# Kernel tuning notes

Measured on AMD Instinct MI355X. Metric: run time of the kernel, lower is better.

## Reference

```python
import jax, jax.numpy as jnp
from jax import lax
import numpy as np

B, L_IN, C_IN, C_MARK = 4, 1024, 7, 4
D, H, DK, DFF, NL = 512, 8, 64, 2048, 4
WINDOW = [4, 4, 4]
INNER = 5


def _get_mask(input_size, window_size, inner_size):
    all_size = [input_size]
    for w in window_size:
        all_size.append(all_size[-1] // w)
    L = sum(all_size)
    m = np.zeros((L, L), dtype=np.float32)
    iw = inner_size // 2
    for li in range(len(all_size)):
        start = sum(all_size[:li])
        for i in range(start, start + all_size[li]):
            m[i, max(i - iw, start):min(i + iw + 1, start + all_size[li])] = 1
    for li in range(1, len(all_size)):
        start = sum(all_size[:li])
        for i in range(start, start + all_size[li]):
            ls = start - all_size[li - 1] + (i - start) * window_size[li - 1]
            if i == start + all_size[li] - 1:
                rs = start
            else:
                rs = start - all_size[li - 1] + (i - start + 1) * window_size[li - 1]
            m[i, ls:rs] = 1
            m[ls:rs, i] = 1
    return (1 - m).astype(bool), all_size


def _refer_points(all_sizes, window_size):
    n = all_sizes[0]
    idx = np.zeros((n, len(all_sizes)), dtype=np.int64)
    for i in range(n):
        idx[i, 0] = i
        former = i
        for j in range(1, len(all_sizes)):
            start = sum(all_sizes[:j])
            inner = former - (start - all_sizes[j - 1])
            former = start + min(inner // window_size[j - 1], all_sizes[j] - 1)
            idx[i, j] = former
    return idx


def _pos_emb(L, d):
    pos = np.arange(L, dtype=np.float32)[:, None]
    div = np.exp(np.arange(0, d, 2, dtype=np.float32) * (-np.log(10000.0) / d))
    pe = np.zeros((L, d), dtype=np.float32)
    pe[:, 0::2] = np.sin(pos * div)
    pe[:, 1::2] = np.cos(pos * div)
    return pe


def _ln(x, g, b, eps=1e-5):
    mu = x.mean(-1, keepdims=True)
    v = ((x - mu) ** 2).mean(-1, keepdims=True)
    return (x - mu) * lax.rsqrt(v + eps) * g + b


def setup_inputs() -> dict:
    key = jax.random.key(0)
    ks = iter(jax.random.split(key, 64))

    def nrm(shape, fan_in):
        return jax.random.normal(next(ks), shape, jnp.float32) / np.float32(np.sqrt(fan_in))

    return dict(
        x_enc=jax.random.normal(next(ks), (B, L_IN, C_IN), jnp.float32),
        x_mark=jax.random.uniform(next(ks), (B, L_IN, C_MARK), jnp.float32),
        conv_w=nrm((D, C_IN, 3), C_IN * 3), conv_b=jnp.zeros((D,), jnp.float32),
        temp_w=nrm((C_MARK, D), C_MARK), temp_b=jnp.zeros((D,), jnp.float32),
        down_w=nrm((D, DK), D), down_b=jnp.zeros((DK,), jnp.float32),
        pyr_conv_w=nrm((3, DK, DK, WINDOW[0]), DK * WINDOW[0]),
        pyr_conv_b=jnp.zeros((3, DK), jnp.float32),
        bn_g=jnp.ones((3, DK), jnp.float32), bn_b=jnp.zeros((3, DK), jnp.float32),
        up_w=nrm((DK, D), DK), up_b=jnp.zeros((D,), jnp.float32),
        norm_g=jnp.ones((D,), jnp.float32), norm_b=jnp.zeros((D,), jnp.float32),
        wq=nrm((NL, D, H * DK), D), wk=nrm((NL, D, H * DK), D), wv=nrm((NL, D, H * DK), D),
        fc_w=nrm((NL, H * DK, D), H * DK), fc_b=jnp.zeros((NL, D), jnp.float32),
        ln1_g=jnp.ones((NL, D), jnp.float32), ln1_b=jnp.zeros((NL, D), jnp.float32),
        w1=nrm((NL, D, DFF), D), b1=jnp.zeros((NL, DFF), jnp.float32),
        w2=nrm((NL, DFF, D), DFF), b2=jnp.zeros((NL, D), jnp.float32),
        ln2_g=jnp.ones((NL, D), jnp.float32), ln2_b=jnp.zeros((NL, D), jnp.float32),
    )


def reference(x_enc, x_mark, conv_w, conv_b, temp_w, temp_b, down_w, down_b,
              pyr_conv_w, pyr_conv_b, bn_g, bn_b, up_w, up_b, norm_g, norm_b,
              wq, wk, wv, fc_w, fc_b, ln1_g, ln1_b, w1, b1, w2, b2, ln2_g, ln2_b):
    mask_np, all_size = _get_mask(L_IN, WINDOW, INNER)
    mask = jnp.asarray(mask_np)                      # (L_tot, L_tot) bool, True = blocked
    idx = jnp.asarray(_refer_points(all_size, WINDOW))  # (L_IN, n_levels)
    pe = jnp.asarray(_pos_emb(L_IN, D))
    L_tot = sum(all_size)

    # --- DataEmbedding: circular Conv1d token emb + positional + temporal linear ---
    xt = jnp.transpose(x_enc, (0, 2, 1))             # (B, C_IN, L)
    xt = jnp.concatenate([xt[:, :, -1:], xt, xt[:, :, :1]], axis=-1)  # circular pad=1
    val = lax.conv_general_dilated(xt, conv_w, (1,), 'VALID',
                                   dimension_numbers=('NCH', 'OIH', 'NCH'))
    val = jnp.transpose(val, (0, 2, 1)) + conv_b
    seq = val + pe[None] + x_mark @ temp_w + temp_b  # (B, L_IN, D); dropout = eval no-op

    # --- Bottleneck_Construct: build pyramid levels with strided convs ---
    tmp = jnp.transpose(seq @ down_w + down_b, (0, 2, 1))  # (B, DK, L_IN)
    outs = []
    for i in range(len(WINDOW)):
        tmp = lax.conv_general_dilated(tmp, pyr_conv_w[i], (WINDOW[i],), 'VALID',
                                       dimension_numbers=('NCH', 'OIH', 'NCH'))
        tmp = tmp + pyr_conv_b[i][None, :, None]
        # BatchNorm1d at eval with running stats (0,1): affine only
        tmp = jax.nn.elu(tmp * bn_g[i][None, :, None] + bn_b[i][None, :, None])
        outs.append(tmp)
    pyr = jnp.transpose(jnp.concatenate(outs, axis=2), (0, 2, 1)) @ up_w + up_b
    seq = _ln(jnp.concatenate([seq, pyr], axis=1), norm_g, norm_b)  # (B, L_tot, D)

    temperature = float(np.sqrt(DK))
    for l in range(NL):
        # post-norm multi-head attention with pyramidal boolean mask
        res = seq
        q = (seq @ wq[l]).reshape(B, L_tot, H, DK)
        k = (seq @ wk[l]).reshape(B, L_tot, H, DK)
        v = (seq @ wv[l]).reshape(B, L_tot, H, DK)
        att = jnp.einsum('bqhd,bkhd->bhqk', q / temperature, k)
        att = jnp.where(mask[None, None], jnp.float32(-1e9), att)
        p = jax.nn.softmax(att, axis=-1)
        o = jnp.einsum('bhqk,bkhd->bqhd', p, v).reshape(B, L_tot, H * DK)
        seq = _ln(o @ fc_w[l] + fc_b[l] + res, ln1_g[l], ln1_b[l])
        # post-norm FFN (exact gelu, as F.gelu)
        res = seq
        hmid = jax.nn.gelu(seq @ w1[l] + b1[l], approximate=False)
        seq = _ln(hmid @ w2[l] + b2[l] + res, ln2_g[l], ln2_b[l])

    # --- refer_points gather: concat all pyramid levels per input position ---
    out = seq[:, idx, :]                             # (B, L_IN, n_levels, D)
    return out.reshape(B, L_IN, -1)                  # (B, L_IN, n_levels*D)
```

## Files before the change

### kernel.cpp

```cpp
#include <hip/hip_runtime.h>
#include <hip/hip_bf16.h>
#include <math.h>


typedef __attribute__((ext_vector_type(8))) short short8;
typedef __attribute__((ext_vector_type(4))) float f32x4;

__device__ inline ushort f2bf(float x) {
  union { __hip_bfloat16 h; ushort u; } cv; cv.h = __float2bfloat16(x); return cv.u;
}
__device__ inline float bf2f(ushort u) {
  union { unsigned int i; float f; } cv; cv.i = (unsigned)u << 16; return cv.f;
}
__device__ inline float lo16(unsigned u) { union { unsigned i; float f; } c; c.i = u << 16; return c.f; }
__device__ inline float hi16(unsigned u) { union { unsigned i; float f; } c; c.i = u & 0xffff0000u; return c.f; }
__device__ inline unsigned pack2(float a, float b) {
  return (unsigned)f2bf(a) | ((unsigned)f2bf(b) << 16);
}

__device__ inline float gelu_f(float x) {
  float y = 0.7978845608028654f * (x + 0.044715f * x * x * x);
  float t = __expf(-2.0f * y);
  float th = (1.0f - t) / (1.0f + t);
  return 0.5f * x * (1.0f + th);
}

__device__ inline int xcd_chunk(int orig, int nwg) {
  int q = nwg >> 3, r = nwg & 7;
  int xcd = orig & 7, idx = orig >> 3;
  int base = (xcd < r) ? xcd * (q + 1) : r * (q + 1) + (xcd - r) * q;
  return base + idx;
}

#define GLD16(gp, lp)                                                        \
  __builtin_amdgcn_global_load_lds(                                          \
      (const __attribute__((address_space(1))) void*)(gp),                   \
      (__attribute__((address_space(3))) void*)(lp), 16, 0, 0)

__global__ __launch_bounds__(512) void embed_kernel(
    const float* __restrict__ x_enc, const float* __restrict__ x_mark,
    const float* __restrict__ conv_w, const float* __restrict__ conv_b,
    const float* __restrict__ temp_w, const float* __restrict__ temp_b,
    float* __restrict__ e) {
  int bl = blockIdx.x;
  int b = bl >> 10, l = bl & 1023;
  int d = threadIdx.x;
  int lm1 = (l + 1023) & 1023;
  int lp1 = (l + 1) & 1023;
  const float* w  = conv_w + d * 21;
  const float* x0 = x_enc + (size_t)(b * 1024 + lm1) * 7;
  const float* x1 = x_enc + (size_t)(b * 1024 + l)   * 7;
  const float* x2 = x_enc + (size_t)(b * 1024 + lp1) * 7;
  float acc = conv_b[d];
#pragma unroll
  for (int ci = 0; ci < 7; ci++) {
    acc = fmaf(x0[ci], w[ci * 3 + 0], acc);
    acc = fmaf(x1[ci], w[ci * 3 + 1], acc);
    acc = fmaf(x2[ci], w[ci * 3 + 2], acc);
  }
  int j = d >> 1;
  float dv = expf((float)(2 * j) * (-9.210340371976184f / 512.0f));
  float ang = (float)l * dv;
  float pe = (d & 1) ? cosf(ang) : sinf(ang);
  const float* xm = x_mark + (size_t)(b * 1024 + l) * 4;
  float mk = temp_b[d];
  mk = fmaf(xm[0], temp_w[d],        mk);
  mk = fmaf(xm[1], temp_w[512 + d],  mk);
  mk = fmaf(xm[2], temp_w[1024 + d], mk);
  mk = fmaf(xm[3], temp_w[1536 + d], mk);
  e[(size_t)bl * 512 + d] = acc + pe + mk;
}

__global__ __launch_bounds__(256) void transpose_cast(
    const float* __restrict__ src, ushort* __restrict__ dst,
    int K, int N, size_t src_lstride, size_t dst_lstride) {
  src += (size_t)blockIdx.z * src_lstride;
  dst += (size_t)blockIdx.z * dst_lstride;
  __shared__ float t[32][33];
  int k0 = blockIdx.y * 32, n0 = blockIdx.x * 32;
  int tx = threadIdx.x, ty = threadIdx.y;
#pragma unroll
  for (int i = 0; i < 4; i++)
    t[ty + i * 8][tx] = src[(size_t)(k0 + ty + i * 8) * N + n0 + tx];
  __syncthreads();
#pragma unroll
  for (int i = 0; i < 4; i++)
    dst[(size_t)(n0 + ty + i * 8) * K + k0 + tx] = f2bf(t[tx][ty + i * 8]);
}

__global__ __launch_bounds__(256) void gemm_bf16_t64(
    const ushort* __restrict__ A, const ushort* __restrict__ Bt,
    const float* __restrict__ bias, ushort* __restrict__ C,
    int N, int K, int act) {
  __shared__ short As[2][4096];
  __shared__ short Bs[2][4096];
  int nbx = N >> 6;
  int wgid = xcd_chunk(blockIdx.x, gridDim.x);
  int bx = wgid % nbx, by = wgid / nbx;
  int tid = threadIdx.x;
  int w = tid >> 6, lane = tid & 63;
  int bm = by << 6, bn = bx << 6;
  int gch = (tid & 7) ^ ((tid >> 3) & 7);
  const short* Ab = (const short*)A + (size_t)(bm + (tid >> 3)) * K + gch * 8;
  const short* Bb = (const short*)Bt + (size_t)(bn + (tid >> 3)) * K + gch * 8;
  int ldst = (tid & 192) * 8;
  int wr = (w >> 1) << 5, wc = (w & 1) << 5;
  int lr = lane & 15, kg = lane >> 4;
  int cs0 = ((kg)     ^ (lane & 7)) * 8;
  int cs1 = ((4 + kg) ^ (lane & 7)) * 8;
  f32x4 acc[2][2] = {};
#define STG64(buf, kt) do {                                                  \
    GLD16(Ab + (kt),                  &As[buf][ldst]);                       \
    GLD16(Ab + (kt) + (size_t)32 * K, &As[buf][2048 + ldst]);                \
    GLD16(Bb + (kt),                  &Bs[buf][ldst]);                       \
    GLD16(Bb + (kt) + (size_t)32 * K, &Bs[buf][2048 + ldst]); } while (0)
  STG64(0, 0);
  __syncthreads();
  int nt = K >> 6;
  for (int t = 0; t < nt; t++) {
    int cur = t & 1;
    if (t + 1 < nt) STG64(cur ^ 1, (t + 1) << 6);
    short8 a_[2][2], b_[2][2];
#pragma unroll
    for (int m = 0; m < 2; m++) {
      int rb = (wr + m * 16 + lr) * 64;
      a_[m][0] = *(const short8*)&As[cur][rb + cs0];
      a_[m][1] = *(const short8*)&As[cur][rb + cs1];
    }
#pragma unroll
    for (int n = 0; n < 2; n++) {
      int rb = (wc + n * 16 + lr) * 64;
      b_[n][0] = *(const short8*)&Bs[cur][rb + cs0];
      b_[n][1] = *(const short8*)&Bs[cur][rb + cs1];
    }
#pragma unroll
    for (int ks = 0; ks < 2; ks++)
#pragma unroll
      for (int m = 0; m < 2; m++)
#pragma unroll
        for (int n = 0; n < 2; n++)
          acc[m][n] = __builtin_amdgcn_mfma_f32_16x16x32_bf16(a_[m][ks], b_[n][ks], acc[m][n], 0, 0, 0);
    __syncthreads();
  }
#undef STG64
  int r0 = bm + wr + kg * 4;
  int c0 = bn + wc + lr;
#pragma unroll
  for (int m = 0; m < 2; m++) {
#pragma unroll
    for (int n = 0; n < 2; n++) {
      int col = c0 + n * 16;
      float bv = bias ? bias[col] : 0.0f;
#pragma unroll
      for (int j = 0; j < 4; j++) {
        int row = r0 + m * 16 + j;
        float v = acc[m][n][j] + bv;
        if (act == 1) v = gelu_f(v);
        C[(size_t)row * N + col] = f2bf(v);
      }
    }
  }
}

__global__ __launch_bounds__(256) void gemm_bf16_t32(
    const ushort* __restrict__ A, const ushort* __restrict__ Bt,
    const float* __restrict__ bias, ushort* __restrict__ C,
    int N, int K) {
  __shared__ short As[2][2048];
  __shared__ short Bs[2][4096];
  int nbx = N >> 6;
  int wgid = xcd_chunk(blockIdx.x, gridDim.x);
  int bx = wgid % nbx, by = wgid / nbx;
  int tid = threadIdx.x;
  int w = tid >> 6, lane = tid & 63;
  int bm = by << 5, bn = bx << 6;
  int gch = (tid & 7) ^ ((tid >> 3) & 7);
  const short* Ab = (const short*)A + (size_t)(bm + (tid >> 3)) * K + gch * 8;
  const short* Bb = (const short*)Bt + (size_t)(bn + (tid >> 3)) * K + gch * 8;
  int ldst = (tid & 192) * 8;
  int wr = (w >> 1) << 4, wc = (w & 1) << 5;
  int lr = lane & 15, kg = lane >> 4;
  int cs0 = ((kg)     ^ (lane & 7)) * 8;
  int cs1 = ((4 + kg) ^ (lane & 7)) * 8;
  f32x4 acc[2] = {};
#define STG32(buf, kt) do {                                                  \
    GLD16(Ab + (kt),                  &As[buf][ldst]);                       \
    GLD16(Bb + (kt),                  &Bs[buf][ldst]);                       \
    GLD16(Bb + (kt) + (size_t)32 * K, &Bs[buf][2048 + ldst]); } while (0)
  STG32(0, 0);
  __syncthreads();
  int nt = K >> 6;
  for (int t = 0; t < nt; t++) {
    int cur = t & 1;
    if (t + 1 < nt) STG32(cur ^ 1, (t + 1) << 6);
    short8 a_[2], b_[2][2];
    {
      int rb = (wr + lr) * 64;
      a_[0] = *(const short8*)&As[cur][rb + cs0];
      a_[1] = *(const short8*)&As[cur][rb + cs1];
    }
#pragma unroll
    for (int n = 0; n < 2; n++) {
      int rb = (wc + n * 16 + lr) * 64;
      b_[n][0] = *(const short8*)&Bs[cur][rb + cs0];
      b_[n][1] = *(const short8*)&Bs[cur][rb + cs1];
    }
#pragma unroll
    for (int ks = 0; ks < 2; ks++)
#pragma unroll
      for (int n = 0; n < 2; n++)
        acc[n] = __builtin_amdgcn_mfma_f32_16x16x32_bf16(a_[ks], b_[n][ks], acc[n], 0, 0, 0);
    __syncthreads();
  }
#undef STG32
  int r0 = bm + wr + kg * 4;
  int c0 = bn + wc + lr;
#pragma unroll
  for (int n = 0; n < 2; n++) {
    int col = c0 + n * 16;
    float bv = bias ? bias[col] : 0.0f;
#pragma unroll
    for (int j = 0; j < 4; j++) {
      int row = r0 + j;
      C[(size_t)row * N + col] = f2bf(acc[n][j] + bv);
    }
  }
}

__global__ __launch_bounds__(256) void down_gemm(
    const float* __restrict__ A, const float* __restrict__ B,
    const float* __restrict__ bias, float* __restrict__ C) {
  int wgid = xcd_chunk(blockIdx.x, gridDim.x);
  int r0 = wgid << 4;
  int tid = threadIdx.x;
  int col = tid & 63, rq = tid >> 6;
  __shared__ float As[16][32];
  __shared__ float Bs[32][64];
  float acc0 = 0, acc1 = 0, acc2 = 0, acc3 = 0;
  for (int kt = 0; kt < 512; kt += 32) {
    {
      int e = tid * 2;
      int ar = e >> 5, ak = e & 31;
      *(float2*)&As[ar][ak] = *(const float2*)&A[(size_t)(r0 + ar) * 512 + kt + ak];
    }
    {
      int e = tid * 8;
      int br = e >> 6, bc = e & 63;
      *(float4*)&Bs[br][bc]     = *(const float4*)&B[(size_t)(kt + br) * 64 + bc];
      *(float4*)&Bs[br][bc + 4] = *(const float4*)&B[(size_t)(kt + br) * 64 + bc + 4];
    }
    __syncthreads();
#pragma unroll
    for (int kk = 0; kk < 32; kk++) {
      float bv = Bs[kk][col];
      acc0 = fmaf(As[rq][kk],      bv, acc0);
      acc1 = fmaf(As[rq + 4][kk],  bv, acc1);
      acc2 = fmaf(As[rq + 8][kk],  bv, acc2);
      acc3 = fmaf(As[rq + 12][kk], bv, acc3);
    }
    __syncthreads();
  }
  float bv = bias[col];
  C[(size_t)(r0 + rq) * 64 + col]      = acc0 + bv;
  C[(size_t)(r0 + rq + 4) * 64 + col]  = acc1 + bv;
  C[(size_t)(r0 + rq + 8) * 64 + col]  = acc2 + bv;
  C[(size_t)(r0 + rq + 12) * 64 + col] = acc3 + bv;
}

__global__ __launch_bounds__(256) void gemm_f32(
    const float* __restrict__ A, const float* __restrict__ B,
    const float* __restrict__ bias, float* __restrict__ C,
    int M, int N, int K) {
  __shared__ float As[16][68];
  __shared__ float Bs[16][64];
  int tid = threadIdx.x;
  int tx = tid & 15, ty = tid >> 4;
  int bm = blockIdx.y << 6, bn = blockIdx.x << 6;
  const float* Ab = A + (size_t)bm * K;
  const float* Bb = B + bn;
  float acc[4][4] = {};
  for (int kt = 0; kt < K; kt += 16) {
#pragma unroll
    for (int r = 0; r < 4; r++) {
      int e2 = r * 256 + tid;
      As[e2 & 15][e2 >> 4] = Ab[(size_t)(e2 >> 4) * K + kt + (e2 & 15)];
    }
#pragma unroll
    for (int r = 0; r < 4; r++) {
      int e2 = r * 256 + tid;
      Bs[e2 >> 6][e2 & 63] = Bb[(size_t)(kt + (e2 >> 6)) * N + (e2 & 63)];
    }
    __syncthreads();
#pragma unroll
    for (int kk = 0; kk < 16; kk++) {
      float a0 = As[kk][(ty << 2) + 0], a1 = As[kk][(ty << 2) + 1];
      float a2 = As[kk][(ty << 2) + 2], a3 = As[kk][(ty << 2) + 3];
      float b0 = Bs[kk][(tx << 2) + 0], b1 = Bs[kk][(tx << 2) + 1];
      float b2 = Bs[kk][(tx << 2) + 2], b3 = Bs[kk][(tx << 2) + 3];
      acc[0][0] = fmaf(a0, b0, acc[0][0]); acc[0][1] = fmaf(a0, b1, acc[0][1]);
      acc[0][2] = fmaf(a0, b2, acc[0][2]); acc[0][3] = fmaf(a0, b3, acc[0][3]);
      acc[1][0] = fmaf(a1, b0, acc[1][0]); acc[1][1] = fmaf(a1, b1, acc[1][1]);
      acc[1][2] = fmaf(a1, b2, acc[1][2]); acc[1][3] = fmaf(a1, b3, acc[1][3]);
      acc[2][0] = fmaf(a2, b0, acc[2][0]); acc[2][1] = fmaf(a2, b1, acc[2][1]);
      acc[2][2] = fmaf(a2, b2, acc[2][2]); acc[2][3] = fmaf(a2, b3, acc[2][3]);
      acc[3][0] = fmaf(a3, b0, acc[3][0]); acc[3][1] = fmaf(a3, b1, acc[3][1]);
      acc[3][2] = fmaf(a3, b2, acc[3][2]); acc[3][3] = fmaf(a3, b3, acc[3][3]);
    }
    __syncthreads();
  }
#pragma unroll
  for (int i2 = 0; i2 < 4; i2++) {
    int row = bm + (ty << 2) + i2;
#pragma unroll
    for (int j2 = 0; j2 < 4; j2++) {
      int col = bn + (tx << 2) + j2;
      C[(size_t)row * N + col] = acc[i2][j2] + (bias ? bias[col] : 0.0f);
    }
  }
}

__global__ __launch_bounds__(64) void pyr_conv(
    const float* __restrict__ in, int in_base, int in_bstr,
    float* __restrict__ out, int out_base, int out_bstr, int out_len,
    const float* __restrict__ w, const float* __restrict__ bias,
    const float* __restrict__ bng, const float* __restrict__ bnb) {
  int blk = blockIdx.x;
  int b = blk / out_len, to = blk - b * out_len;
  int co = threadIdx.x;
  __shared__ float xin[4][64];
  const float* src = in + (size_t)(b * in_bstr + in_base + 4 * to) * 64;
#pragma unroll
  for (int r2 = 0; r2 < 4; r2++) xin[r2][co] = src[r2 * 64 + co];
  __syncthreads();
  const float* wr = w + (size_t)co * 256;
  float acc = bias[co];
#pragma unroll 16
  for (int ci = 0; ci < 64; ci++) {
    acc = fmaf(xin[0][ci], wr[ci * 4 + 0], acc);
    acc = fmaf(xin[1][ci], wr[ci * 4 + 1], acc);
    acc = fmaf(xin[2][ci], wr[ci * 4 + 2], acc);
    acc = fmaf(xin[3][ci], wr[ci * 4 + 3], acc);
  }
  float y = fmaf(bng[co], acc, bnb[co]);
  y = y > 0.0f ? y : expm1f(y);
  out[(size_t)(b * out_bstr + out_base + to) * 64 + co] = y;
}

__global__ __launch_bounds__(256) void ln_concat(
    const float* __restrict__ e, const float* __restrict__ pyru,
    const float* __restrict__ g, const float* __restrict__ bta,
    ushort* __restrict__ seq_bf) {
  int r = (blockIdx.x << 2) + (threadIdx.x >> 6);
  int lane = threadIdx.x & 63;
  int b = r / 1360, i = r - b * 1360;
  const float* src = (i < 1024)
      ? (e    + (size_t)(b * 1024 + i) * 512)
      : (pyru + (size_t)(b * 336 + (i - 1024)) * 512);
  int c = lane << 3;
  float4 v0 = *(const float4*)&src[c];
  float4 v1 = *(const float4*)&src[c + 4];
  float sum = v0.x + v0.y + v0.z + v0.w + v1.x + v1.y + v1.z + v1.w;
#pragma unroll
  for (int off = 1; off < 64; off <<= 1) sum += __shfl_xor(sum, off);
  float mu = sum * (1.0f / 512.0f);
  float d[8] = { v0.x - mu, v0.y - mu, v0.z - mu, v0.w - mu,
                 v1.x - mu, v1.y - mu, v1.z - mu, v1.w - mu };
  float sq = d[0]*d[0] + d[1]*d[1] + d[2]*d[2] + d[3]*d[3]
           + d[4]*d[4] + d[5]*d[5] + d[6]*d[6] + d[7]*d[7];
#pragma unroll
  for (int off = 1; off < 64; off <<= 1) sq += __shfl_xor(sq, off);
  float inv = rsqrtf(sq * (1.0f / 512.0f) + 1e-5f);
  float4 g0 = *(const float4*)&g[c],   g1 = *(const float4*)&g[c + 4];
  float4 b0 = *(const float4*)&bta[c], b1 = *(const float4*)&bta[c + 4];
  uint4 pk;
  pk.x = pack2(d[0]*inv*g0.x + b0.x, d[1]*inv*g0.y + b0.y);
  pk.y = pack2(d[2]*inv*g0.z + b0.z, d[3]*inv*g0.w + b0.w);
  pk.z = pack2(d[4]*inv*g1.x + b1.x, d[5]*inv*g1.y + b1.y);
  pk.w = pack2(d[6]*inv*g1.z + b1.z, d[7]*inv*g1.w + b1.w);
  *(uint4*)(seq_bf + (size_t)r * 512 + c) = pk;
}

__global__ __launch_bounds__(256) void ln_add(
    ushort* __restrict__ seq_bf, const ushort* __restrict__ t1,
    const float* __restrict__ g, const float* __restrict__ bta) {
  int r = (blockIdx.x << 2) + (threadIdx.x >> 6);
  int lane = threadIdx.x & 63;
  int c = lane << 3;
  ushort* row = seq_bf + (size_t)r * 512 + c;
  uint4 sv = *(const uint4*)row;
  uint4 tv = *(const uint4*)(t1 + (size_t)r * 512 + c);
  float v[8] = {
    lo16(sv.x) + lo16(tv.x), hi16(sv.x) + hi16(tv.x),
    lo16(sv.y) + lo16(tv.y), hi16(sv.y) + hi16(tv.y),
    lo16(sv.z) + lo16(tv.z), hi16(sv.z) + hi16(tv.z),
    lo16(sv.w) + lo16(tv.w), hi16(sv.w) + hi16(tv.w) };
  float sum = v[0]+v[1]+v[2]+v[3]+v[4]+v[5]+v[6]+v[7];
#pragma unroll
  for (int off = 1; off < 64; off <<= 1) sum += __shfl_xor(sum, off);
  float mu = sum * (1.0f / 512.0f);
  float sq = 0.0f;
#pragma unroll
  for (int k = 0; k < 8; k++) { v[k] -= mu; sq += v[k] * v[k]; }
#pragma unroll
  for (int off = 1; off < 64; off <<= 1) sq += __shfl_xor(sq, off);
  float inv = rsqrtf(sq * (1.0f / 512.0f) + 1e-5f);
  float4 g0 = *(const float4*)&g[c],   g1 = *(const float4*)&g[c + 4];
  float4 b0 = *(const float4*)&bta[c], b1 = *(const float4*)&bta[c + 4];
  uint4 pk;
  pk.x = pack2(v[0]*inv*g0.x + b0.x, v[1]*inv*g0.y + b0.y);
  pk.y = pack2(v[2]*inv*g0.z + b0.z, v[3]*inv*g0.w + b0.w);
  pk.z = pack2(v[4]*inv*g1.x + b1.x, v[5]*inv*g1.y + b1.y);
  pk.w = pack2(v[6]*inv*g1.z + b1.z, v[7]*inv*g1.w + b1.w);
  *(uint4*)row = pk;
}

__global__ __launch_bounds__(512) void attn_sparse(
    const ushort* __restrict__ qkv, ushort* __restrict__ o) {
  int r = blockIdx.x;
  int b = r / 1360, i = r - b * 1360;
  int h = threadIdx.x >> 6, lane = threadIdx.x & 63;
  int S, sz, li;
  if (i < 1024)      { li = 0; S = 0;    sz = 1024; }
  else if (i < 1280) { li = 1; S = 1024; sz = 256; }
  else if (i < 1344) { li = 2; S = 1280; sz = 64; }
  else               { li = 3; S = 1344; sz = 16; }
  int p = i - S;
  int lo = p - 2; if (lo < 0) lo = 0;
  int hi = p + 2; if (hi > sz - 1) hi = sz - 1;
  int cnt = hi - lo + 1;
  int nk = cnt + (li > 0 ? 4 : 0) + (li < 3 ? 1 : 0);
  int Sprev = (li == 1) ? 0 : (li == 2) ? 1024 : 1280;
  int Snext = (li == 0) ? 1024 : (li == 1) ? 1280 : 1344;
  int j2 = lane >> 2, c = lane & 3;
  int key;
  if (j2 < cnt)                      key = S + lo + j2;
  else if (li > 0 && j2 - cnt < 4)   key = Sprev + 4 * p + (j2 - cnt);
  else if (li < 3)                   key = Snext + (p >> 2);
  else                               key = S + p;
  float partial = 0.0f;
  {
    const uint4* qv = (const uint4*)(qkv + (size_t)r * 1536 + h * 64 + c * 16);
    const uint4* kv = (const uint4*)(qkv + (size_t)(b * 1360 + key) * 1536 + 512 + h * 64 + c * 16);
#pragma unroll
    for (int cc = 0; cc < 2; cc++) {
      uint4 a = qv[cc], k4 = kv[cc];
      partial = fmaf(lo16(a.x), lo16(k4.x), partial); partial = fmaf(hi16(a.x), hi16(k4.x), partial);
      partial = fmaf(lo16(a.y), lo16(k4.y), partial); partial = fmaf(hi16(a.y), hi16(k4.y), partial);
      partial = fmaf(lo16(a.z), lo16(k4.z), partial); partial = fmaf(hi16(a.z), hi16(k4.z), partial);
      partial = fmaf(lo16(a.w), lo16(k4.w), partial); partial = fmaf(hi16(a.w), hi16(k4.w), partial);
    }
  }
  partial += __shfl_xor(partial, 1);
  partial += __shfl_xor(partial, 2);
  float s = partial * 0.125f;
  float m = -1e30f;
  for (int j = 0; j < nk; j++) m = fmaxf(m, __shfl(s, 4 * j));
  float denom = 0.0f;
  for (int j = 0; j < nk; j++) denom += __expf(__shfl(s, 4 * j) - m);
  float inv = 1.0f / denom;
  float acc = 0.0f;
  for (int j = 0; j < nk; j++) {
    float pj = __expf(__shfl(s, 4 * j) - m) * inv;
    int kj = __shfl(key, 4 * j);
    float vv = bf2f(qkv[(size_t)(b * 1360 + kj) * 1536 + 1024 + h * 64 + lane]);
    acc = fmaf(pj, vv, acc);
  }
  o[(size_t)r * 512 + h * 64 + lane] = f2bf(acc);
}

__global__ __launch_bounds__(512) void gather_out(
    const ushort* __restrict__ seq_bf, float* __restrict__ out) {
  int bl = blockIdx.x;
  int b = bl >> 10, i = bl & 1023;
  int d = threadIdx.x;
  size_t ob = (size_t)bl * 2048 + d;
  size_t base = (size_t)b * 1360;
  out[ob]        = bf2f(seq_bf[(base + i) * 512 + d]);
  out[ob + 512]  = bf2f(seq_bf[(base + 1024 + (i >> 2)) * 512 + d]);
  out[ob + 1024] = bf2f(seq_bf[(base + 1280 + (i >> 4)) * 512 + d]);
  out[ob + 1536] = bf2f(seq_bf[(base + 1344 + (i >> 6)) * 512 + d]);
}

extern "C" void kernel_launch(void* const* d_in, const int* in_sizes, int n_in,
                              void* d_out, int out_size, void* d_ws, size_t ws_size,
                              hipStream_t stream) {
  const float* x_enc   = (const float*)d_in[0];
  const float* x_mark  = (const float*)d_in[1];
  const float* conv_w  = (const float*)d_in[2];
  const float* conv_b  = (const float*)d_in[3];
  const float* temp_w  = (const float*)d_in[4];
  const float* temp_b  = (const float*)d_in[5];
  const float* down_w  = (const float*)d_in[6];
  const float* down_b  = (const float*)d_in[7];
  const float* pyr_w   = (const float*)d_in[8];
  const float* pyr_b   = (const float*)d_in[9];
  const float* bn_g    = (const float*)d_in[10];
  const float* bn_b    = (const float*)d_in[11];
  const float* up_w    = (const float*)d_in[12];
  const float* up_b    = (const float*)d_in[13];
  const float* norm_g  = (const float*)d_in[14];
  const float* norm_b  = (const float*)d_in[15];
  const float* wq      = (const float*)d_in[16];
  const float* wk      = (const float*)d_in[17];
  const float* wv      = (const float*)d_in[18];
  const float* fc_w    = (const float*)d_in[19];
  const float* fc_b    = (const float*)d_in[20];
  const float* ln1_g   = (const float*)d_in[21];
  const float* ln1_b   = (const float*)d_in[22];
  const float* w1      = (const float*)d_in[23];
  const float* b1      = (const float*)d_in[24];
  const float* w2      = (const float*)d_in[25];
  const float* b2      = (const float*)d_in[26];
  const float* ln2_g   = (const float*)d_in[27];
  const float* ln2_b   = (const float*)d_in[28];

  float* ws = (float*)d_ws;
  float*  e      = ws;
  float*  tmp0   = ws + 2097152;
  float*  pyrf   = ws + 2359296;
  float*  pyru   = ws + 2445312;
  ushort* qkv_bf = (ushort*)ws;
  ushort* o_bf   = (ushort*)(ws + 4227072);
  ushort* th_bf  = (ushort*)ws;
  ushort* t1     = (ushort*)(ws + 5636096);
  ushort* seq_bf = (ushort*)(ws + 11272192);
  ushort* qkvw   = (ushort*)(ws + 12681216);
  ushort* fcw    = (ushort*)(ws + 14254080);
  ushort* w1t    = (ushort*)(ws + 14778368);
  ushort* w2t    = (ushort*)(ws + 16875520);

  dim3 tb(32, 8);
  transpose_cast<<<dim3(16, 16, 4), tb, 0, stream>>>(wq, qkvw,          512, 512,  262144, 786432);
  transpose_cast<<<dim3(16, 16, 4), tb, 0, stream>>>(wk, qkvw + 262144, 512, 512,  262144, 786432);
  transpose_cast<<<dim3(16, 16, 4), tb, 0, stream>>>(wv, qkvw + 524288, 512, 512,  262144, 786432);
  transpose_cast<<<dim3(16, 16, 4), tb, 0, stream>>>(fc_w, fcw,         512, 512,  262144, 262144);
  transpose_cast<<<dim3(64, 16, 4), tb, 0, stream>>>(w1, w1t,           512, 2048, 1048576, 1048576);
  transpose_cast<<<dim3(16, 64, 4), tb, 0, stream>>>(w2, w2t,           2048, 512, 1048576, 1048576);

  embed_kernel<<<4096, 512, 0, stream>>>(x_enc, x_mark, conv_w, conv_b,
                                         temp_w, temp_b, e);
  down_gemm<<<256, 256, 0, stream>>>(e, down_w, down_b, tmp0);
  pyr_conv<<<4 * 256, 64, 0, stream>>>(tmp0, 0, 1024, pyrf, 0, 336, 256,
                                       pyr_w, pyr_b, bn_g, bn_b);
  pyr_conv<<<4 * 64, 64, 0, stream>>>(pyrf, 0, 336, pyrf, 256, 336, 64,
                                      pyr_w + 16384, pyr_b + 64, bn_g + 64, bn_b + 64);
  pyr_conv<<<4 * 16, 64, 0, stream>>>(pyrf, 256, 336, pyrf, 320, 336, 16,
                                      pyr_w + 32768, pyr_b + 128, bn_g + 128, bn_b + 128);
  gemm_f32<<<dim3(8, 21), 256, 0, stream>>>(pyrf, up_w, up_b, pyru, 1344, 512, 64);
  ln_concat<<<1360, 256, 0, stream>>>(e, pyru, norm_g, norm_b, seq_bf);

  for (int l = 0; l < 4; l++) {
    gemm_bf16_t64<<<24 * 86, 256, 0, stream>>>(seq_bf, qkvw + (size_t)l * 786432,
                                               nullptr, qkv_bf, 1536, 512, 0);
    attn_sparse<<<5440, 512, 0, stream>>>(qkv_bf, o_bf);
    gemm_bf16_t32<<<8 * 172, 256, 0, stream>>>(o_bf, fcw + (size_t)l * 262144,
                                               fc_b + l * 512, t1, 512, 512);
    ln_add<<<1360, 256, 0, stream>>>(seq_bf, t1, ln1_g + l * 512, ln1_b + l * 512);
    gemm_bf16_t64<<<32 * 86, 256, 0, stream>>>(seq_bf, w1t + (size_t)l * 1048576,
                                               b1 + l * 2048, th_bf, 2048, 512, 1);
    gemm_bf16_t32<<<8 * 172, 256, 0, stream>>>(th_bf, w2t + (size_t)l * 1048576,
                                               b2 + l * 512, t1, 512, 2048);
    ln_add<<<1360, 256, 0, stream>>>(seq_bf, t1, ln2_g + l * 512, ln2_b + l * 512);
  }
  gather_out<<<4096, 512, 0, stream>>>(seq_bf, (float*)d_out);
}
```

Baseline: 566.9 us.

## Move pyramid down/up projections to bf16 MFMA GEMMs with bf16 intermediates

Replaces the scalar fp32 down-projection and up-projection GEMMs with the existing bf16 MFMA GEMM kernel. The embedding kernel now also emits a bf16 copy, the pyramid conv stages read and write bf16, and two extra transpose-cast launches prepare the small weights. This removes slow FP32 CUDA-core GEMMs and halves intermediate traffic in the pyramid branch, at the cost of bf16 precision in that branch and two more small launches.

After: 541.8 us. 1.05x faster.

```diff
diff --git a/kernel.cpp b/kernel.cpp
--- a/kernel.cpp
+++ b/kernel.cpp
@@ -41,7 +41,7 @@
     const float* __restrict__ x_enc, const float* __restrict__ x_mark,
     const float* __restrict__ conv_w, const float* __restrict__ conv_b,
     const float* __restrict__ temp_w, const float* __restrict__ temp_b,
-    float* __restrict__ e) {
+    float* __restrict__ e, ushort* __restrict__ e_bf) {
   int bl = blockIdx.x;
   int b = bl >> 10, l = bl & 1023;
   int d = threadIdx.x;
@@ -68,7 +68,9 @@
   mk = fmaf(xm[1], temp_w[512 + d],  mk);
   mk = fmaf(xm[2], temp_w[1024 + d], mk);
   mk = fmaf(xm[3], temp_w[1536 + d], mk);
-  e[(size_t)bl * 512 + d] = acc + pe + mk;
+  float v = acc + pe + mk;
+  e[(size_t)bl * 512 + d] = v;
+  e_bf[(size_t)bl * 512 + d] = f2bf(v);
 }
 
 __global__ __launch_bounds__(256) void transpose_cast(
@@ -227,110 +229,18 @@
   }
 }
 
-__global__ __launch_bounds__(256) void down_gemm(
-    const float* __restrict__ A, const float* __restrict__ B,
-    const float* __restrict__ bias, float* __restrict__ C) {
-  int wgid = xcd_chunk(blockIdx.x, gridDim.x);
-  int r0 = wgid << 4;
-  int tid = threadIdx.x;
-  int col = tid & 63, rq = tid >> 6;
-  __shared__ float As[16][32];
-  __shared__ float Bs[32][64];
-  float acc0 = 0, acc1 = 0, acc2 = 0, acc3 = 0;
-  for (int kt = 0; kt < 512; kt += 32) {
-    {
-      int e = tid * 2;
-      int ar = e >> 5, ak = e & 31;
-      *(float2*)&As[ar][ak] = *(const float2*)&A[(size_t)(r0 + ar) * 512 + kt + ak];
-    }
-    {
-      int e = tid * 8;
-      int br = e >> 6, bc = e & 63;
-      *(float4*)&Bs[br][bc]     = *(const float4*)&B[(size_t)(kt + br) * 64 + bc];
-      *(float4*)&Bs[br][bc + 4] = *(const float4*)&B[(size_t)(kt + br) * 64 + bc + 4];
-    }
-    __syncthreads();
-#pragma unroll
-    for (int kk = 0; kk < 32; kk++) {
-      float bv = Bs[kk][col];
-      acc0 = fmaf(As[rq][kk],      bv, acc0);
-      acc1 = fmaf(As[rq + 4][kk],  bv, acc1);
-      acc2 = fmaf(As[rq + 8][kk],  bv, acc2);
-      acc3 = fmaf(As[rq + 12][kk], bv, acc3);
-    }
-    __syncthreads();
-  }
-  float bv = bias[col];
-  C[(size_t)(r0 + rq) * 64 + col]      = acc0 + bv;
-  C[(size_t)(r0 + rq + 4) * 64 + col]  = acc1 + bv;
-  C[(size_t)(r0 + rq + 8) * 64 + col]  = acc2 + bv;
-  C[(size_t)(r0 + rq + 12) * 64 + col] = acc3 + bv;
-}
-
-__global__ __launch_bounds__(256) void gemm_f32(
-    const float* __restrict__ A, const float* __restrict__ B,
-    const float* __restrict__ bias, float* __restrict__ C,
-    int M, int N, int K) {
-  __shared__ float As[16][68];
-  __shared__ float Bs[16][64];
-  int tid = threadIdx.x;
-  int tx = tid & 15, ty = tid >> 4;
-  int bm = blockIdx.y << 6, bn = blockIdx.x << 6;
-  const float* Ab = A + (size_t)bm * K;
-  const float* Bb = B + bn;
-  float acc[4][4] = {};
-  for (int kt = 0; kt < K; kt += 16) {
-#pragma unroll
-    for (int r = 0; r < 4; r++) {
-      int e2 = r * 256 + tid;
-      As[e2 & 15][e2 >> 4] = Ab[(size_t)(e2 >> 4) * K + kt + (e2 & 15)];
-    }
-#pragma unroll
-    for (int r = 0; r < 4; r++) {
-      int e2 = r * 256 + tid;
-      Bs[e2 >> 6][e2 & 63] = Bb[(size_t)(kt + (e2 >> 6)) * N + (e2 & 63)];
-    }
-    __syncthreads();
-#pragma unroll
-    for (int kk = 0; kk < 16; kk++) {
-      float a0 = As[kk][(ty << 2) + 0], a1 = As[kk][(ty << 2) + 1];
-      float a2 = As[kk][(ty << 2) + 2], a3 = As[kk][(ty << 2) + 3];
-      float b0 = Bs[kk][(tx << 2) + 0], b1 = Bs[kk][(tx << 2) + 1];
-      float b2 = Bs[kk][(tx << 2) + 2], b3 = Bs[kk][(tx << 2) + 3];
-      acc[0][0] = fmaf(a0, b0, acc[0][0]); acc[0][1] = fmaf(a0, b1, acc[0][1]);
-      acc[0][2] = fmaf(a0, b2, acc[0][2]); acc[0][3] = fmaf(a0, b3, acc[0][3]);
-      acc[1][0] = fmaf(a1, b0, acc[1][0]); acc[1][1] = fmaf(a1, b1, acc[1][1]);
-      acc[1][2] = fmaf(a1, b2, acc[1][2]); acc[1][3] = fmaf(a1, b3, acc[1][3]);
-      acc[2][0] = fmaf(a2, b0, acc[2][0]); acc[2][1] = fmaf(a2, b1, acc[2][1]);
-      acc[2][2] = fmaf(a2, b2, acc[2][2]); acc[2][3] = fmaf(a2, b3, acc[2][3]);
-      acc[3][0] = fmaf(a3, b0, acc[3][0]); acc[3][1] = fmaf(a3, b1, acc[3][1]);
-      acc[3][2] = fmaf(a3, b2, acc[3][2]); acc[3][3] = fmaf(a3, b3, acc[3][3]);
-    }
-    __syncthreads();
-  }
-#pragma unroll
-  for (int i2 = 0; i2 < 4; i2++) {
-    int row = bm + (ty << 2) + i2;
-#pragma unroll
-    for (int j2 = 0; j2 < 4; j2++) {
-      int col = bn + (tx << 2) + j2;
-      C[(size_t)row * N + col] = acc[i2][j2] + (bias ? bias[col] : 0.0f);
-    }
-  }
-}
-
 __global__ __launch_bounds__(64) void pyr_conv(
-    const float* __restrict__ in, int in_base, int in_bstr,
-    float* __restrict__ out, int out_base, int out_bstr, int out_len,
+    const ushort* __restrict__ in, int in_base, int in_bstr,
+    ushort* __restrict__ out, int out_base, int out_bstr, int out_len,
     const float* __restrict__ w, const float* __restrict__ bias,
     const float* __restrict__ bng, const float* __restrict__ bnb) {
   int blk = blockIdx.x;
   int b = blk / out_len, to = blk - b * out_len;
   int co = threadIdx.x;
   __shared__ float xin[4][64];
-  const float* src = in + (size_t)(b * in_bstr + in_base + 4 * to) * 64;
-#pragma unroll
-  for (int r2 = 0; r2 < 4; r2++) xin[r2][co] = src[r2 * 64 + co];
+  const ushort* src = in + (size_t)(b * in_bstr + in_base + 4 * to) * 64;
+#pragma unroll
+  for (int r2 = 0; r2 < 4; r2++) xin[r2][co] = bf2f(src[r2 * 64 + co]);
   __syncthreads();
   const float* wr = w + (size_t)co * 256;
   float acc = bias[co];
@@ -343,40 +253,46 @@
   }
   float y = fmaf(bng[co], acc, bnb[co]);
   y = y > 0.0f ? y : expm1f(y);
-  out[(size_t)(b * out_bstr + out_base + to) * 64 + co] = y;
+  out[(size_t)(b * out_bstr + out_base + to) * 64 + co] = f2bf(y);
 }
 
 __global__ __launch_bounds__(256) void ln_concat(
-    const float* __restrict__ e, const float* __restrict__ pyru,
+    const float* __restrict__ e, const ushort* __restrict__ pyru,
     const float* __restrict__ g, const float* __restrict__ bta,
     ushort* __restrict__ seq_bf) {
   int r = (blockIdx.x << 2) + (threadIdx.x >> 6);
   int lane = threadIdx.x & 63;
   int b = r / 1360, i = r - b * 1360;
-  const float* src = (i < 1024)
-      ? (e    + (size_t)(b * 1024 + i) * 512)
-      : (pyru + (size_t)(b * 336 + (i - 1024)) * 512);
   int c = lane << 3;
-  float4 v0 = *(const float4*)&src[c];
-  float4 v1 = *(const float4*)&src[c + 4];
-  float sum = v0.x + v0.y + v0.z + v0.w + v1.x + v1.y + v1.z + v1.w;
+  float v[8];
+  if (i < 1024) {
+    const float* src = e + (size_t)(b * 1024 + i) * 512 + c;
+    float4 v0 = *(const float4*)&src[0];
+    float4 v1 = *(const float4*)&src[4];
+    v[0] = v0.x; v[1] = v0.y; v[2] = v0.z; v[3] = v0.w;
+    v[4] = v1.x; v[5] = v1.y; v[6] = v1.z; v[7] = v1.w;
+  } else {
+    uint4 sv = *(const uint4*)(pyru + (size_t)(b * 336 + (i - 1024)) * 512 + c);
+    v[0] = lo16(sv.x); v[1] = hi16(sv.x); v[2] = lo16(sv.y); v[3] = hi16(sv.y);
+    v[4] = lo16(sv.z); v[5] = hi16(sv.z); v[6] = lo16(sv.w); v[7] = hi16(sv.w);
+  }
+  float sum = v[0]+v[1]+v[2]+v[3]+v[4]+v[5]+v[6]+v[7];
 #pragma unroll
   for (int off = 1; off < 64; off <<= 1) sum += __shfl_xor(sum, off);
   float mu = sum * (1.0f / 512.0f);
-  float d[8] = { v0.x - mu, v0.y - mu, v0.z - mu, v0.w - mu,
-                 v1.x - mu, v1.y - mu, v1.z - mu, v1.w - mu };
-  float sq = d[0]*d[0] + d[1]*d[1] + d[2]*d[2] + d[3]*d[3]
-           + d[4]*d[4] + d[5]*d[5] + d[6]*d[6] + d[7]*d[7];
+  float sq = 0.0f;
+#pragma unroll
+  for (int k = 0; k < 8; k++) { v[k] -= mu; sq += v[k] * v[k]; }
 #pragma unroll
   for (int off = 1; off < 64; off <<= 1) sq += __shfl_xor(sq, off);
   float inv = rsqrtf(sq * (1.0f / 512.0f) + 1e-5f);
   float4 g0 = *(const float4*)&g[c],   g1 = *(const float4*)&g[c + 4];
   float4 b0 = *(const float4*)&bta[c], b1 = *(const float4*)&bta[c + 4];
   uint4 pk;
-  pk.x = pack2(d[0]*inv*g0.x + b0.x, d[1]*inv*g0.y + b0.y);
-  pk.y = pack2(d[2]*inv*g0.z + b0.z, d[3]*inv*g0.w + b0.w);
-  pk.z = pack2(d[4]*inv*g1.x + b1.x, d[5]*inv*g1.y + b1.y);
-  pk.w = pack2(d[6]*inv*g1.z + b1.z, d[7]*inv*g1.w + b1.w);
+  pk.x = pack2(v[0]*inv*g0.x + b0.x, v[1]*inv*g0.y + b0.y);
+  pk.y = pack2(v[2]*inv*g0.z + b0.z, v[3]*inv*g0.w + b0.w);
+  pk.z = pack2(v[4]*inv*g1.x + b1.x, v[5]*inv*g1.y + b1.y);
+  pk.w = pack2(v[6]*inv*g1.z + b1.z, v[7]*inv*g1.w + b1.w);
   *(uint4*)(seq_bf + (size_t)r * 512 + c) = pk;
 }
 
@@ -515,14 +431,17 @@
   const float* ln2_b   = (const float*)d_in[28];
 
   float* ws = (float*)d_ws;
-  float*  e      = ws;
-  float*  tmp0   = ws + 2097152;
-  float*  pyrf   = ws + 2359296;
-  float*  pyru   = ws + 2445312;
+  float*  e       = ws;
+  ushort* e_bf    = (ushort*)(ws + 2097152);
+  ushort* tmp0_bf = (ushort*)(ws + 3145728);
+  ushort* pyrf_bf = (ushort*)(ws + 3276800);
+  ushort* pyru_bf = (ushort*)(ws + 3319808);
   ushort* qkv_bf = (ushort*)ws;
   ushort* o_bf   = (ushort*)(ws + 4227072);
   ushort* th_bf  = (ushort*)ws;
   ushort* t1     = (ushort*)(ws + 5636096);
+  ushort* dwt    = (ushort*)(ws + 7045120);
+  ushort* uwt    = (ushort*)(ws + 7061504);
   ushort* seq_bf = (ushort*)(ws + 11272192);
   ushort* qkvw   = (ushort*)(ws + 12681216);
   ushort* fcw    = (ushort*)(ws + 14254080);
@@ -536,18 +455,20 @@
   transpose_cast<<<dim3(16, 16, 4), tb, 0, stream>>>(fc_w, fcw,         512, 512,  262144, 262144);
   transpose_cast<<<dim3(64, 16, 4), tb, 0, stream>>>(w1, w1t,           512, 2048, 1048576, 1048576);
   transpose_cast<<<dim3(16, 64, 4), tb, 0, stream>>>(w2, w2t,           2048, 512, 1048576, 1048576);
+  transpose_cast<<<dim3(2, 16, 1), tb, 0, stream>>>(down_w, dwt,        512, 64,   0, 0);
+  transpose_cast<<<dim3(16, 2, 1), tb, 0, stream>>>(up_w, uwt,          64, 512,   0, 0);
 
   embed_kernel<<<4096, 512, 0, stream>>>(x_enc, x_mark, conv_w, conv_b,
-                                         temp_w, temp_b, e);
-  down_gemm<<<256, 256, 0, stream>>>(e, down_w, down_b, tmp0);
-  pyr_conv<<<4 * 256, 64, 0, stream>>>(tmp0, 0, 1024, pyrf, 0, 336, 256,
+                                         temp_w, temp_b, e, e_bf);
+  gemm_bf16_t32<<<128, 256, 0, stream>>>(e_bf, dwt, down_b, tmp0_bf, 64, 512);
+  pyr_conv<<<4 * 256, 64, 0, stream>>>(tmp0_bf, 0, 1024, pyrf_bf, 0, 336, 256,
                                        pyr_w, pyr_b, bn_g, bn_b);
-  pyr_conv<<<4 * 64, 64, 0, stream>>>(pyrf, 0, 336, pyrf, 256, 336, 64,
+  pyr_conv<<<4 * 64, 64, 0, stream>>>(pyrf_bf, 0, 336, pyrf_bf, 256, 336, 64,
                                       pyr_w + 16384, pyr_b + 64, bn_g + 64, bn_b + 64);
-  pyr_conv<<<4 * 16, 64, 0, stream>>>(pyrf, 256, 336, pyrf, 320, 336, 16,
+  pyr_conv<<<4 * 16, 64, 0, stream>>>(pyrf_bf, 256, 336, pyrf_bf, 320, 336, 16,
                                       pyr_w + 32768, pyr_b + 128, bn_g + 128, bn_b + 128);
-  gemm_f32<<<dim3(8, 21), 256, 0, stream>>>(pyrf, up_w, up_b, pyru, 1344, 512, 64);
-  ln_concat<<<1360, 256, 0, stream>>>(e, pyru, norm_g, norm_b, seq_bf);
+  gemm_bf16_t32<<<8 * 42, 256, 0, stream>>>(pyrf_bf, uwt, up_b, pyru_bf, 512, 64);
+  ln_concat<<<1360, 256, 0, stream>>>(e, pyru_bf, norm_g, norm_b, seq_bf);
 
   for (int l = 0; l < 4; l++) {
     gemm_bf16_t64<<<24 * 86, 256, 0, stream>>>(seq_bf, qkvw + (size_t)l * 786432,
```
